# Optimization experiments

Hardware: AMD Instinct MI355X
Metric: run time of the kernel (lower is better)

The kernel has to match this reference:

```python
import jax, jax.numpy as jnp
import numpy as np

D_MODEL = 1024
NUM_HEADS = 16
D_K = D_MODEL // NUM_HEADS


def setup_inputs() -> dict:
    key = jax.random.key(0)
    ks = jax.random.split(key, 11)
    B, S = 4, 2048
    s = 1.0 / np.sqrt(D_MODEL)
    inp = {
        "q": jax.random.normal(ks[0], (B, S, D_MODEL), jnp.float32),
        "k": jax.random.normal(ks[1], (B, S, D_MODEL), jnp.float32),
        "v": jax.random.normal(ks[2], (B, S, D_MODEL), jnp.float32),
        "Wq": jax.random.normal(ks[3], (D_MODEL, D_MODEL), jnp.float32) * s,
        "bq": jnp.zeros((D_MODEL,), jnp.float32),
        "Wk": jax.random.normal(ks[4], (D_MODEL, D_MODEL), jnp.float32) * s,
        "bk": jnp.zeros((D_MODEL,), jnp.float32),
        "Wv": jax.random.normal(ks[5], (D_MODEL, D_MODEL), jnp.float32) * s,
        "bv": jnp.zeros((D_MODEL,), jnp.float32),
        "Wo": jax.random.normal(ks[6], (D_MODEL, D_MODEL), jnp.float32) * s,
        "bo": jnp.zeros((D_MODEL,), jnp.float32),
    }
    return inp


def reference(q, k, v, Wq, bq, Wk, bk, Wv, bv, Wo, bo):
    B, S, _ = q.shape
    # QKV projections, then split heads: [B,S,D] -> [B,H,S,d_k]
    def split_heads(x):
        return x.reshape(B, -1, NUM_HEADS, D_K).transpose(0, 2, 1, 3)
    Q = split_heads(q @ Wq + bq)
    K = split_heads(k @ Wk + bk)
    V = split_heads(v @ Wv + bv)
    # scaled dot-product attention (mask=None, dropout p=0 -> identity)
    scores = jnp.einsum("bhqd,bhkd->bhqk", Q, K) / jnp.sqrt(jnp.float32(D_K))
    attn = jax.nn.softmax(scores, axis=-1)
    out = jnp.einsum("bhqk,bhkd->bhqd", attn, V)
    out = out.transpose(0, 2, 1, 3).reshape(B, -1, D_MODEL)
    return out @ Wo + bo
```

## Files before the change

kernel.cpp:

```cpp
#include <hip/hip_runtime.h>

#define MB (1ull << 20)

typedef __attribute__((ext_vector_type(8))) short bf16x8;
typedef __attribute__((ext_vector_type(4))) float f32x4;

#if defined(__has_builtin)
#if __has_builtin(__builtin_amdgcn_global_load_lds)
#define HAS_GLL 1
#endif
#endif
#ifndef HAS_GLL
#define HAS_GLL 0
#endif

__device__ __forceinline__ unsigned short f2bf(float f) {
  unsigned u = __float_as_uint(f);
  u += 0x7fffu + ((u >> 16) & 1u);
  return (unsigned short)(u >> 16);
}

#if HAS_GLL
__device__ __forceinline__ void gl16(const unsigned short* g, unsigned short* l) {
  __builtin_amdgcn_global_load_lds((const __attribute__((address_space(1))) void*)g,
                                   (__attribute__((address_space(3))) void*)l, 16, 0, 0);
}
#endif

__global__ __launch_bounds__(256) void cvt3(const float* __restrict__ x0,
                                            const float* __restrict__ x1,
                                            const float* __restrict__ x2,
                                            unsigned short* __restrict__ y0,
                                            unsigned short* __restrict__ y1,
                                            unsigned short* __restrict__ y2, int n) {
  const int z = blockIdx.y;
  const float* x = (z == 0) ? x0 : (z == 1) ? x1 : x2;
  unsigned short* y = (z == 0) ? y0 : (z == 1) ? y1 : y2;
  int i = (blockIdx.x * 256 + threadIdx.x) * 4;
  if (i >= n) return;
  float4 v = *(const float4*)(x + i);
  uint2 p;
  p.x = (unsigned)f2bf(v.x) | ((unsigned)f2bf(v.y) << 16);
  p.y = (unsigned)f2bf(v.z) | ((unsigned)f2bf(v.w) << 16);
  *(uint2*)(y + i) = p;
}

__global__ __launch_bounds__(256) void transpose4(const float* __restrict__ W0,
                                                  const float* __restrict__ W1,
                                                  const float* __restrict__ W2,
                                                  const float* __restrict__ W3,
                                                  unsigned short* __restrict__ T0,
                                                  unsigned short* __restrict__ T1,
                                                  unsigned short* __restrict__ T2,
                                                  unsigned short* __restrict__ T3) {
  const int z = blockIdx.z;
  const float* W = (z == 0) ? W0 : (z == 1) ? W1 : (z == 2) ? W2 : W3;
  unsigned short* WT = (z == 0) ? T0 : (z == 1) ? T1 : (z == 2) ? T2 : T3;
  __shared__ float tile[32][33];
  int bx = blockIdx.x * 32;
  int by = blockIdx.y * 32;
  int tx = threadIdx.x & 31, ty = threadIdx.x >> 5;
#pragma unroll
  for (int i = 0; i < 32; i += 8)
    tile[ty + i][tx] = W[(by + ty + i) * 1024 + bx + tx];
  __syncthreads();
#pragma unroll
  for (int i = 0; i < 32; i += 8)
    WT[(bx + ty + i) * 1024 + by + tx] = f2bf(tile[tx][ty + i]);
}

__device__ __forceinline__ void gemm_core(const unsigned short* __restrict__ A,
                                          const unsigned short* __restrict__ Bt, int K, int m0,
                                          int n0, unsigned short* As, unsigned short* Bs,
                                          f32x4 (&acc)[4][4]) {
  const int tid = threadIdx.x;
  const int wave = tid >> 6, lane = tid & 63;
  const int quad = lane >> 4, r = lane & 15;
  const int wm = (wave >> 1) * 64, wn = (wave & 1) * 64;

  const int srow8 = tid >> 3;
  const int clog8 = ((tid & 7) ^ (srow8 & 7)) * 8;
  const unsigned short* Ag = A + (size_t)(m0 + srow8) * K + clog8;
  const unsigned short* Bg = Bt + (size_t)(n0 + srow8) * K + clog8;

  const int cA = ((0 ^ quad) ^ (r & 7)) * 8;
  const int cB = ((4 ^ quad) ^ (r & 7)) * 8;

  for (int k0 = 0; k0 < K; k0 += 64) {
    __syncthreads();
#if HAS_GLL
#pragma unroll
    for (int s = 0; s < 4; ++s) {
      gl16(Ag + (size_t)(s * 32) * K + k0, As + s * 2048 + tid * 8);
      gl16(Bg + (size_t)(s * 32) * K + k0, Bs + s * 2048 + tid * 8);
    }
#else
#pragma unroll
    for (int s = 0; s < 4; ++s) {
      uint4 a = *(const uint4*)(Ag + (size_t)(s * 32) * K + k0);
      uint4 b = *(const uint4*)(Bg + (size_t)(s * 32) * K + k0);
      *(uint4*)(As + s * 2048 + tid * 8) = a;
      *(uint4*)(Bs + s * 2048 + tid * 8) = b;
    }
#endif
    __syncthreads();
#pragma unroll
    for (int ks = 0; ks < 2; ++ks) {
      const int co = ks ? cB : cA;
      bf16x8 af[4], bfr[4];
#pragma unroll
      for (int i = 0; i < 4; ++i) af[i] = *(const bf16x8*)(As + (wm + i * 16 + r) * 64 + co);
#pragma unroll
      for (int j = 0; j < 4; ++j) bfr[j] = *(const bf16x8*)(Bs + (wn + j * 16 + r) * 64 + co);
#pragma unroll
      for (int i = 0; i < 4; ++i)
#pragma unroll
        for (int j = 0; j < 4; ++j)
          acc[i][j] = __builtin_amdgcn_mfma_f32_16x16x32_bf16(af[i], bfr[j], acc[i][j], 0, 0, 0);
    }
  }
}

__global__ __launch_bounds__(256) void gemm_qkv(
    const unsigned short* __restrict__ A0, const unsigned short* __restrict__ A1,
    const unsigned short* __restrict__ A2, const unsigned short* __restrict__ B0,
    const unsigned short* __restrict__ B1, const unsigned short* __restrict__ B2,
    const float* __restrict__ b0, const float* __restrict__ b1, const float* __restrict__ b2,
    unsigned short* __restrict__ O0, unsigned short* __restrict__ O1,
    unsigned short* __restrict__ O2, int M, int N, int K, float scaleQ) {
  __shared__ __align__(16) unsigned short As[128 * 64];
  __shared__ __align__(16) unsigned short Bs[128 * 64];
  const int z = blockIdx.z;
  const unsigned short* A = (z == 0) ? A0 : (z == 1) ? A1 : A2;
  const unsigned short* Bt = (z == 0) ? B0 : (z == 1) ? B1 : B2;
  const float* bias = (z == 0) ? b0 : (z == 1) ? b1 : b2;
  const float scale = (z == 0) ? scaleQ : 1.0f;
  const int m0 = blockIdx.y * 128, n0 = blockIdx.x * 128;

  f32x4 acc[4][4] = {};
  gemm_core(A, Bt, K, m0, n0, As, Bs, acc);

  const int lane = threadIdx.x & 63, wave = threadIdx.x >> 6;
  const int quad = lane >> 4, r = lane & 15;
  const int wm = (wave >> 1) * 64, wn = (wave & 1) * 64;

  if (z < 2) {
    unsigned short* Cout = (z == 0) ? O0 : O1;
#pragma unroll
    for (int i = 0; i < 4; ++i)
#pragma unroll
      for (int j = 0; j < 4; ++j) {
        const int col = n0 + wn + j * 16 + r;
        const float bv = bias[col];
#pragma unroll
        for (int t = 0; t < 4; ++t) {
          const int row = m0 + wm + i * 16 + quad * 4 + t;
          Cout[(size_t)row * N + col] = f2bf((acc[i][j][t] + bv) * scale);
        }
      }
  } else {
    const int b = m0 >> 11;
#pragma unroll
    for (int i = 0; i < 4; ++i)
#pragma unroll
      for (int j = 0; j < 4; ++j) {
        const int col = n0 + wn + j * 16 + r;
        const float bv = bias[col];
        const int rloc = (m0 & 2047) + wm + i * 16 + quad * 4;
        uint2 u;
        u.x = ((unsigned)f2bf(acc[i][j][1] + bv) << 16) | f2bf(acc[i][j][0] + bv);
        u.y = ((unsigned)f2bf(acc[i][j][3] + bv) << 16) | f2bf(acc[i][j][2] + bv);
        *(uint2*)(O2 + ((size_t)(b * N + col)) * 2048 + rloc) = u;
      }
  }
}

__global__ __launch_bounds__(256) void gemm_o(const unsigned short* __restrict__ A,
                                              const unsigned short* __restrict__ Bt,
                                              const float* __restrict__ bias,
                                              float* __restrict__ Cout, int M, int N, int K) {
  __shared__ __align__(16) unsigned short As[128 * 64];
  __shared__ __align__(16) unsigned short Bs[128 * 64];
  const int m0 = blockIdx.y * 128, n0 = blockIdx.x * 128;
  f32x4 acc[4][4] = {};
  gemm_core(A, Bt, K, m0, n0, As, Bs, acc);

  const int lane = threadIdx.x & 63, wave = threadIdx.x >> 6;
  const int quad = lane >> 4, r = lane & 15;
  const int wm = (wave >> 1) * 64, wn = (wave & 1) * 64;
#pragma unroll
  for (int i = 0; i < 4; ++i)
#pragma unroll
    for (int j = 0; j < 4; ++j) {
      const int col = n0 + wn + j * 16 + r;
      const float bv = bias[col];
#pragma unroll
      for (int t = 0; t < 4; ++t) {
        const int row = m0 + wm + i * 16 + quad * 4 + t;
        Cout[(size_t)row * N + col] = acc[i][j][t] + bv;
      }
    }
}

__global__ __launch_bounds__(256) void flash_mfma(const unsigned short* __restrict__ Qb,
                                                  const unsigned short* __restrict__ Kb,
                                                  const unsigned short* __restrict__ Vt,
                                                  unsigned short* __restrict__ Ob) {
  __shared__ __align__(16) unsigned short Ksh[64 * 64];
  __shared__ __align__(16) unsigned short Vts[64 * 64];
  __shared__ __align__(16) unsigned short Ps[4 * 16 * 64];
  const int tid = threadIdx.x;
  const int wave = tid >> 6, lane = tid & 63;
  const int quad = lane >> 4, r = lane & 15;
  const int b = blockIdx.y >> 4, h = blockIdx.y & 15;
  const int qbase = b * 2048 + blockIdx.x * 256 + wave * 64;

  bf16x8 qf[4][2];
#pragma unroll
  for (int jq = 0; jq < 4; ++jq)
#pragma unroll
    for (int ks = 0; ks < 2; ++ks)
      qf[jq][ks] = *(const bf16x8*)(Qb + (size_t)(qbase + jq * 16 + r) * 1024 + h * 64 +
                                    ks * 32 + quad * 8);

  f32x4 oacc[4][4] = {};
  float lp[4] = {0.f, 0.f, 0.f, 0.f};

  const int srow = tid >> 2;
  const int c0 = (tid & 3) * 2;
  const int c0p = c0 ^ (srow & 7);
  const unsigned short* Kg = Kb + (size_t)(b * 2048 + srow) * 1024 + h * 64 + c0 * 8;
  const unsigned short* Vg = Vt + (size_t)(b * 1024 + h * 64 + srow) * 2048 + c0 * 8;
  unsigned short* PsW = Ps + wave * 1024;
  const int rx = (r & 7);

  for (int kt0 = 0; kt0 < 32; ++kt0) {
    uint4 ka = *(const uint4*)Kg;
    uint4 kb2 = *(const uint4*)(Kg + 8);
    uint4 va = *(const uint4*)Vg;
    uint4 vb2 = *(const uint4*)(Vg + 8);
    Kg += 64 * 1024;
    Vg += 64;
    __syncthreads();
    *(uint4*)(Ksh + srow * 64 + c0p * 8) = ka;
    *(uint4*)(Ksh + srow * 64 + (c0p ^ 1) * 8) = kb2;
    *(uint4*)(Vts + srow * 64 + c0p * 8) = va;
    *(uint4*)(Vts + srow * 64 + (c0p ^ 1) * 8) = vb2;
    __syncthreads();

    bf16x8 kf[4][2], vf[4][2];
#pragma unroll
    for (int kt = 0; kt < 4; ++kt)
#pragma unroll
      for (int ks = 0; ks < 2; ++ks) {
        kf[kt][ks] = *(const bf16x8*)(Ksh + (kt * 16 + r) * 64 + (((ks * 4 + quad) ^ rx) * 8));
        vf[kt][ks] = *(const bf16x8*)(Vts + (kt * 16 + r) * 64 + (((ks * 4 + quad) ^ rx) * 8));
      }

#pragma unroll
    for (int jq = 0; jq < 4; ++jq) {
      f32x4 st[4] = {};
#pragma unroll
      for (int ks = 0; ks < 2; ++ks)
#pragma unroll
        for (int kt = 0; kt < 4; ++kt)
          st[kt] = __builtin_amdgcn_mfma_f32_16x16x32_bf16(kf[kt][ks], qf[jq][ks], st[kt], 0, 0, 0);
#pragma unroll
      for (int kt = 0; kt < 4; ++kt) {
        float p0 = __builtin_amdgcn_exp2f(st[kt][0]);
        float p1 = __builtin_amdgcn_exp2f(st[kt][1]);
        float p2 = __builtin_amdgcn_exp2f(st[kt][2]);
        float p3 = __builtin_amdgcn_exp2f(st[kt][3]);
        lp[jq] += (p0 + p1) + (p2 + p3);
        uint2 u;
        u.x = __builtin_amdgcn_perm(__float_as_uint(p1) + 0x8000u,
                                    __float_as_uint(p0) + 0x8000u, 0x07060302u);
        u.y = __builtin_amdgcn_perm(__float_as_uint(p3) + 0x8000u,
                                    __float_as_uint(p2) + 0x8000u, 0x07060302u);
        *(uint2*)(PsW + r * 64 + (((kt * 2 + (quad >> 1)) ^ rx) * 8) + (quad & 1) * 4) = u;
      }
#pragma unroll
      for (int ks = 0; ks < 2; ++ks) {
        bf16x8 pf = *(const bf16x8*)(PsW + r * 64 + (((ks * 4 + quad) ^ rx) * 8));
#pragma unroll
        for (int dt = 0; dt < 4; ++dt)
          oacc[jq][dt] = __builtin_amdgcn_mfma_f32_16x16x32_bf16(vf[dt][ks], pf, oacc[jq][dt], 0, 0, 0);
      }
    }
  }

#pragma unroll
  for (int jq = 0; jq < 4; ++jq) {
    float l = lp[jq];
    l += __shfl_xor(l, 16);
    l += __shfl_xor(l, 32);
    float inv = 1.0f / l;
#pragma unroll
    for (int dt = 0; dt < 4; ++dt) {
      uint2 u;
      u.x = ((unsigned)f2bf(oacc[jq][dt][1] * inv) << 16) | f2bf(oacc[jq][dt][0] * inv);
      u.y = ((unsigned)f2bf(oacc[jq][dt][3] * inv) << 16) | f2bf(oacc[jq][dt][2] * inv);
      *(uint2*)(Ob + (size_t)(qbase + jq * 16 + r) * 1024 + h * 64 + dt * 16 + quad * 4) = u;
    }
  }
}

extern "C" void kernel_launch(void* const* d_in, const int* in_sizes, int n_in, void* d_out,
                              int out_size, void* d_ws, size_t ws_size, hipStream_t stream) {
  const float* q = (const float*)d_in[0];
  const float* k = (const float*)d_in[1];
  const float* v = (const float*)d_in[2];
  const float* Wq = (const float*)d_in[3];
  const float* bq = (const float*)d_in[4];
  const float* Wk = (const float*)d_in[5];
  const float* bk = (const float*)d_in[6];
  const float* Wv = (const float*)d_in[7];
  const float* bv = (const float*)d_in[8];
  const float* Wo = (const float*)d_in[9];
  const float* bo = (const float*)d_in[10];

  unsigned char* ws = (unsigned char*)d_ws;
  unsigned short* qb = (unsigned short*)(ws + 0 * MB);
  unsigned short* kb = (unsigned short*)(ws + 16 * MB);
  unsigned short* vb = (unsigned short*)(ws + 32 * MB);
  unsigned short* WqT = (unsigned short*)(ws + 48 * MB);
  unsigned short* WkT = (unsigned short*)(ws + 50 * MB);
  unsigned short* WvT = (unsigned short*)(ws + 52 * MB);
  unsigned short* WoT = (unsigned short*)(ws + 54 * MB);
  unsigned short* Qb = (unsigned short*)(ws + 56 * MB);
  unsigned short* Kbf = (unsigned short*)(ws + 72 * MB);
  unsigned short* Vtr = (unsigned short*)(ws + 88 * MB);
  unsigned short* AOb = (unsigned short*)(ws + 104 * MB);

  const int M = 8192, D = 1024;
  const float c2 = 0.18033688011112042f;

  cvt3<<<dim3(M * D / 1024, 3), 256, 0, stream>>>(q, k, v, qb, kb, vb, M * D);
  transpose4<<<dim3(32, 32, 4), 256, 0, stream>>>(Wq, Wk, Wv, Wo, WqT, WkT, WvT, WoT);

  gemm_qkv<<<dim3(D / 128, M / 128, 3), 256, 0, stream>>>(qb, kb, vb, WqT, WkT, WvT, bq, bk, bv,
                                                          Qb, Kbf, Vtr, M, D, D, c2);

  flash_mfma<<<dim3(8, 64), 256, 0, stream>>>(Qb, Kbf, Vtr, AOb);

  gemm_o<<<dim3(D / 128, M / 128), 256, 0, stream>>>(AOb, WoT, bo, (float*)d_out, M, D, D);
}
```

Baseline: 393.9 us.

## Load GEMM B fragments directly from global and split flash QK/PV phases

In the shared GEMM core, the B operand is no longer staged through LDS. Each wave loads its B fragments straight from global memory into registers, and the Bs shared buffer is removed. This halves LDS traffic and LDS footprint, possibly raising occupancy, but each wave now issues uncoalesced-ish global loads with no reuse across the two M-waves. In the flash kernel, P for all four query sub-tiles is written to an enlarged per-wave LDS buffer before V fragments are loaded, separating the QK/softmax phase from the PV phase to reduce register pressure, at the cost of a larger Ps buffer (32KB).

```diff
diff --git a/kernel.cpp b/kernel.cpp
--- a/kernel.cpp
+++ b/kernel.cpp
@@ -71,52 +71,52 @@
 
 __device__ __forceinline__ void gemm_core(const unsigned short* __restrict__ A,
                                           const unsigned short* __restrict__ Bt, int K, int m0,
-                                          int n0, unsigned short* As, unsigned short* Bs,
-                                          f32x4 (&acc)[4][4]) {
+                                          int n0, unsigned short* As, f32x4 (&acc)[4][4]) {
   const int tid = threadIdx.x;
   const int wave = tid >> 6, lane = tid & 63;
   const int quad = lane >> 4, r = lane & 15;
   const int wm = (wave >> 1) * 64, wn = (wave & 1) * 64;
+  const int rx = r & 7;
 
   const int srow8 = tid >> 3;
   const int clog8 = ((tid & 7) ^ (srow8 & 7)) * 8;
   const unsigned short* Ag = A + (size_t)(m0 + srow8) * K + clog8;
-  const unsigned short* Bg = Bt + (size_t)(n0 + srow8) * K + clog8;
-
-  const int cA = ((0 ^ quad) ^ (r & 7)) * 8;
-  const int cB = ((4 ^ quad) ^ (r & 7)) * 8;
+  const unsigned short* Bg = Bt + (size_t)(n0 + wn + r) * K + quad * 8;
+
+  const int cA = (quad ^ rx) * 8;
+  const int cB = ((4 ^ quad) ^ rx) * 8;
 
   for (int k0 = 0; k0 < K; k0 += 64) {
     __syncthreads();
 #if HAS_GLL
 #pragma unroll
-    for (int s = 0; s < 4; ++s) {
-      gl16(Ag + (size_t)(s * 32) * K + k0, As + s * 2048 + tid * 8);
-      gl16(Bg + (size_t)(s * 32) * K + k0, Bs + s * 2048 + tid * 8);
-    }
+    for (int s = 0; s < 4; ++s) gl16(Ag + (size_t)(s * 32) * K + k0, As + s * 2048 + tid * 8);
 #else
 #pragma unroll
     for (int s = 0; s < 4; ++s) {
       uint4 a = *(const uint4*)(Ag + (size_t)(s * 32) * K + k0);
-      uint4 b = *(const uint4*)(Bg + (size_t)(s * 32) * K + k0);
       *(uint4*)(As + s * 2048 + tid * 8) = a;
-      *(uint4*)(Bs + s * 2048 + tid * 8) = b;
-    }
-#endif
+    }
+#endif
+    bf16x8 bfr[2][4];
+#pragma unroll
+    for (int ks = 0; ks < 2; ++ks)
+#pragma unroll
+      for (int j = 0; j < 4; ++j)
+        bfr[ks][j] = *(const bf16x8*)(Bg + (size_t)(j * 16) * K + k0 + ks * 32);
     __syncthreads();
 #pragma unroll
     for (int ks = 0; ks < 2; ++ks) {
       const int co = ks ? cB : cA;
-      bf16x8 af[4], bfr[4];
+      bf16x8 af[4];
 #pragma unroll
       for (int i = 0; i < 4; ++i) af[i] = *(const bf16x8*)(As + (wm + i * 16 + r) * 64 + co);
 #pragma unroll
-      for (int j = 0; j < 4; ++j) bfr[j] = *(const bf16x8*)(Bs + (wn + j * 16 + r) * 64 + co);
-#pragma unroll
       for (int i = 0; i < 4; ++i)
 #pragma unroll
         for (int j = 0; j < 4; ++j)
-          acc[i][j] = __builtin_amdgcn_mfma_f32_16x16x32_bf16(af[i], bfr[j], acc[i][j], 0, 0, 0);
+          acc[i][j] =
+              __builtin_amdgcn_mfma_f32_16x16x32_bf16(af[i], bfr[ks][j], acc[i][j], 0, 0, 0);
     }
   }
 }
@@ -129,7 +129,6 @@
     unsigned short* __restrict__ O0, unsigned short* __restrict__ O1,
     unsigned short* __restrict__ O2, int M, int N, int K, float scaleQ) {
   __shared__ __align__(16) unsigned short As[128 * 64];
-  __shared__ __align__(16) unsigned short Bs[128 * 64];
   const int z = blockIdx.z;
   const unsigned short* A = (z == 0) ? A0 : (z == 1) ? A1 : A2;
   const unsigned short* Bt = (z == 0) ? B0 : (z == 1) ? B1 : B2;
@@ -138,7 +137,7 @@
   const int m0 = blockIdx.y * 128, n0 = blockIdx.x * 128;
 
   f32x4 acc[4][4] = {};
-  gemm_core(A, Bt, K, m0, n0, As, Bs, acc);
+  gemm_core(A, Bt, K, m0, n0, As, acc);
 
   const int lane = threadIdx.x & 63, wave = threadIdx.x >> 6;
   const int quad = lane >> 4, r = lane & 15;
@@ -180,10 +179,9 @@
                                               const float* __restrict__ bias,
                                               float* __restrict__ Cout, int M, int N, int K) {
   __shared__ __align__(16) unsigned short As[128 * 64];
-  __shared__ __align__(16) unsigned short Bs[128 * 64];
   const int m0 = blockIdx.y * 128, n0 = blockIdx.x * 128;
   f32x4 acc[4][4] = {};
-  gemm_core(A, Bt, K, m0, n0, As, Bs, acc);
+  gemm_core(A, Bt, K, m0, n0, As, acc);
 
   const int lane = threadIdx.x & 63, wave = threadIdx.x >> 6;
   const int quad = lane >> 4, r = lane & 15;
@@ -208,12 +206,13 @@
                                                   unsigned short* __restrict__ Ob) {
   __shared__ __align__(16) unsigned short Ksh[64 * 64];
   __shared__ __align__(16) unsigned short Vts[64 * 64];
-  __shared__ __align__(16) unsigned short Ps[4 * 16 * 64];
+  __shared__ __align__(16) unsigned short Ps[4 * 64 * 64];
   const int tid = threadIdx.x;
   const int wave = tid >> 6, lane = tid & 63;
   const int quad = lane >> 4, r = lane & 15;
   const int b = blockIdx.y >> 4, h = blockIdx.y & 15;
   const int qbase = b * 2048 + blockIdx.x * 256 + wave * 64;
+  const int rx = r & 7;
 
   bf16x8 qf[4][2];
 #pragma unroll
@@ -231,8 +230,7 @@
   const int c0p = c0 ^ (srow & 7);
   const unsigned short* Kg = Kb + (size_t)(b * 2048 + srow) * 1024 + h * 64 + c0 * 8;
   const unsigned short* Vg = Vt + (size_t)(b * 1024 + h * 64 + srow) * 2048 + c0 * 8;
-  unsigned short* PsW = Ps + wave * 1024;
-  const int rx = (r & 7);
+  unsigned short* PsW = Ps + wave * 4096;
 
   for (int kt0 = 0; kt0 < 32; ++kt0) {
     uint4 ka = *(const uint4*)Kg;
@@ -248,14 +246,12 @@
     *(uint4*)(Vts + srow * 64 + (c0p ^ 1) * 8) = vb2;
     __syncthreads();
 
-    bf16x8 kf[4][2], vf[4][2];
+    bf16x8 kf[4][2];
 #pragma unroll
     for (int kt = 0; kt < 4; ++kt)
 #pragma unroll
-      for (int ks = 0; ks < 2; ++ks) {
+      for (int ks = 0; ks < 2; ++ks)
         kf[kt][ks] = *(const bf16x8*)(Ksh + (kt * 16 + r) * 64 + (((ks * 4 + quad) ^ rx) * 8));
-        vf[kt][ks] = *(const bf16x8*)(Vts + (kt * 16 + r) * 64 + (((ks * 4 + quad) ^ rx) * 8));
-      }
 
 #pragma unroll
     for (int jq = 0; jq < 4; ++jq) {
@@ -277,16 +273,27 @@
                                     __float_as_uint(p0) + 0x8000u, 0x07060302u);
         u.y = __builtin_amdgcn_perm(__float_as_uint(p3) + 0x8000u,
                                     __float_as_uint(p2) + 0x8000u, 0x07060302u);
-        *(uint2*)(PsW + r * 64 + (((kt * 2 + (quad >> 1)) ^ rx) * 8) + (quad & 1) * 4) = u;
-      }
+        *(uint2*)(PsW + (jq * 16 + r) * 64 + (((kt * 2 + (quad >> 1)) ^ rx) * 8) +
+                  (quad & 1) * 4) = u;
+      }
+    }
+
+    bf16x8 vf[4][2];
+#pragma unroll
+    for (int dt = 0; dt < 4; ++dt)
+#pragma unroll
+      for (int ks = 0; ks < 2; ++ks)
+        vf[dt][ks] = *(const bf16x8*)(Vts + (dt * 16 + r) * 64 + (((ks * 4 + quad) ^ rx) * 8));
+#pragma unroll
+    for (int jq = 0; jq < 4; ++jq)
 #pragma unroll
       for (int ks = 0; ks < 2; ++ks) {
-        bf16x8 pf = *(const bf16x8*)(PsW + r * 64 + (((ks * 4 + quad) ^ rx) * 8));
+        bf16x8 pf = *(const bf16x8*)(PsW + (jq * 16 + r) * 64 + (((ks * 4 + quad) ^ rx) * 8));
 #pragma unroll
         for (int dt = 0; dt < 4; ++dt)
-          oacc[jq][dt] = __builtin_amdgcn_mfma_f32_16x16x32_bf16(vf[dt][ks], pf, oacc[jq][dt], 0, 0, 0);
-      }
-    }
+          oacc[jq][dt] =
+              __builtin_amdgcn_mfma_f32_16x16x32_bf16(vf[dt][ks], pf, oacc[jq][dt], 0, 0, 0);
+      }
   }
 
 #pragma unroll
```

Result: slower. 449.6 us (+14.1%).

## Pad LDS rows and split QK/softmax from PV phase in flash kernel

Applied to the files above, without the earlier changes.

Replaces the XOR-swizzled LDS layout for K, V and P with row padding (stride 72 instead of 64) to avoid bank conflicts. It also enlarges each wave's P buffer to hold all 64 query rows, so the QK^T/softmax pass for all four query subtiles finishes before the PV MFMAs run. V fragments are now loaded only after the score phase, which lowers their register lifetime. The cost is more LDS: the P buffer grows from 8 KB to about 36 KB, which may reduce occupancy.

```diff
diff --git a/kernel.cpp b/kernel.cpp
--- a/kernel.cpp
+++ b/kernel.cpp
@@ -206,9 +206,9 @@
                                                   const unsigned short* __restrict__ Kb,
                                                   const unsigned short* __restrict__ Vt,
                                                   unsigned short* __restrict__ Ob) {
-  __shared__ __align__(16) unsigned short Ksh[64 * 64];
-  __shared__ __align__(16) unsigned short Vts[64 * 64];
-  __shared__ __align__(16) unsigned short Ps[4 * 16 * 64];
+  __shared__ __align__(16) unsigned short Ksh[64 * 72];
+  __shared__ __align__(16) unsigned short Vts[64 * 72];
+  __shared__ __align__(16) unsigned short Ps[4 * 64 * 72];
   const int tid = threadIdx.x;
   const int wave = tid >> 6, lane = tid & 63;
   const int quad = lane >> 4, r = lane & 15;
@@ -226,13 +226,10 @@
   f32x4 oacc[4][4] = {};
   float lp[4] = {0.f, 0.f, 0.f, 0.f};
 
-  const int srow = tid >> 2;
-  const int c0 = (tid & 3) * 2;
-  const int c0p = c0 ^ (srow & 7);
-  const unsigned short* Kg = Kb + (size_t)(b * 2048 + srow) * 1024 + h * 64 + c0 * 8;
-  const unsigned short* Vg = Vt + (size_t)(b * 1024 + h * 64 + srow) * 2048 + c0 * 8;
-  unsigned short* PsW = Ps + wave * 1024;
-  const int rx = (r & 7);
+  const int srow = tid >> 2, sc = (tid & 3) * 16;
+  const unsigned short* Kg = Kb + (size_t)(b * 2048 + srow) * 1024 + h * 64 + sc;
+  const unsigned short* Vg = Vt + (size_t)(b * 1024 + h * 64 + srow) * 2048 + sc;
+  unsigned short* PsW = Ps + wave * (64 * 72);
 
   for (int kt0 = 0; kt0 < 32; ++kt0) {
     uint4 ka = *(const uint4*)Kg;
@@ -242,20 +239,18 @@
     Kg += 64 * 1024;
     Vg += 64;
     __syncthreads();
-    *(uint4*)(Ksh + srow * 64 + c0p * 8) = ka;
-    *(uint4*)(Ksh + srow * 64 + (c0p ^ 1) * 8) = kb2;
-    *(uint4*)(Vts + srow * 64 + c0p * 8) = va;
-    *(uint4*)(Vts + srow * 64 + (c0p ^ 1) * 8) = vb2;
+    *(uint4*)(Ksh + srow * 72 + sc) = ka;
+    *(uint4*)(Ksh + srow * 72 + sc + 8) = kb2;
+    *(uint4*)(Vts + srow * 72 + sc) = va;
+    *(uint4*)(Vts + srow * 72 + sc + 8) = vb2;
     __syncthreads();
 
-    bf16x8 kf[4][2], vf[4][2];
+    bf16x8 kf[4][2];
 #pragma unroll
     for (int kt = 0; kt < 4; ++kt)
 #pragma unroll
-      for (int ks = 0; ks < 2; ++ks) {
-        kf[kt][ks] = *(const bf16x8*)(Ksh + (kt * 16 + r) * 64 + (((ks * 4 + quad) ^ rx) * 8));
-        vf[kt][ks] = *(const bf16x8*)(Vts + (kt * 16 + r) * 64 + (((ks * 4 + quad) ^ rx) * 8));
-      }
+      for (int ks = 0; ks < 2; ++ks)
+        kf[kt][ks] = *(const bf16x8*)(Ksh + (kt * 16 + r) * 72 + ks * 32 + quad * 8);
 
 #pragma unroll
     for (int jq = 0; jq < 4; ++jq) {
@@ -277,16 +272,26 @@
                                     __float_as_uint(p0) + 0x8000u, 0x07060302u);
         u.y = __builtin_amdgcn_perm(__float_as_uint(p3) + 0x8000u,
                                     __float_as_uint(p2) + 0x8000u, 0x07060302u);
-        *(uint2*)(PsW + r * 64 + (((kt * 2 + (quad >> 1)) ^ rx) * 8) + (quad & 1) * 4) = u;
-      }
+        *(uint2*)(PsW + (jq * 16 + r) * 72 + kt * 16 + quad * 4) = u;
+      }
+    }
+
+    bf16x8 vf[4][2];
+#pragma unroll
+    for (int dt = 0; dt < 4; ++dt)
+#pragma unroll
+      for (int ks = 0; ks < 2; ++ks)
+        vf[dt][ks] = *(const bf16x8*)(Vts + (dt * 16 + r) * 72 + ks * 32 + quad * 8);
+#pragma unroll
+    for (int jq = 0; jq < 4; ++jq)
 #pragma unroll
       for (int ks = 0; ks < 2; ++ks) {
-        bf16x8 pf = *(const bf16x8*)(PsW + r * 64 + (((ks * 4 + quad) ^ rx) * 8));
+        bf16x8 pf = *(const bf16x8*)(PsW + (jq * 16 + r) * 72 + ks * 32 + quad * 8);
 #pragma unroll
         for (int dt = 0; dt < 4; ++dt)
-          oacc[jq][dt] = __builtin_amdgcn_mfma_f32_16x16x32_bf16(vf[dt][ks], pf, oacc[jq][dt], 0, 0, 0);
-      }
-    }
+          oacc[jq][dt] =
+              __builtin_amdgcn_mfma_f32_16x16x32_bf16(vf[dt][ks], pf, oacc[jq][dt], 0, 0, 0);
+      }
   }
 
 #pragma unroll
```

New measurement: 356.0 us. 1.11x faster.
